# Optimization experiments

Hardware: AMD Instinct MI355X
Metric: run time of the kernel (lower is better)

Reference implementation:

```python
import jax, jax.numpy as jnp
import numpy as np

EMBED_DIM = 1024
HEAD_DIM = 128

def setup_inputs() -> dict:
    key = jax.random.key(0)
    ks = jax.random.split(key, 7)
    B, S = 4, 2048
    x = jax.random.normal(ks[0], (B, S, EMBED_DIM), dtype=jnp.float32)
    # Linear params: weight [embed_dim, head_dim] (applied as x @ W + b), scaled init
    scale = 1.0 / np.sqrt(EMBED_DIM)
    Wq = jax.random.normal(ks[1], (EMBED_DIM, HEAD_DIM), dtype=jnp.float32) * scale
    Wk = jax.random.normal(ks[2], (EMBED_DIM, HEAD_DIM), dtype=jnp.float32) * scale
    Wv = jax.random.normal(ks[3], (EMBED_DIM, HEAD_DIM), dtype=jnp.float32) * scale
    bq = jax.random.normal(ks[4], (HEAD_DIM,), dtype=jnp.float32) * 0.01
    bk = jax.random.normal(ks[5], (HEAD_DIM,), dtype=jnp.float32) * 0.01
    bv = jax.random.normal(ks[6], (HEAD_DIM,), dtype=jnp.float32) * 0.01
    return {"x": x, "Wq": Wq, "bq": bq, "Wk": Wk, "bk": bk, "Wv": Wv, "bv": bv}

def reference(x, Wq, bq, Wk, bk, Wv, bv):
    # x: [B, S, E]
    S = x.shape[1]
    norm = jnp.asarray(HEAD_DIM ** 0.5, x.dtype)
    q = x @ Wq + bq  # [B, S, D]
    k = x @ Wk + bk
    v = x @ Wv + bv
    scores = jnp.einsum('bsd,btd->bst', q, k) / norm  # [B, S, S]
    causal = jnp.tril(jnp.ones((S, S), dtype=bool))
    scores = jnp.where(causal, scores, -jnp.inf)
    att = jax.nn.softmax(scores, axis=-1)
    return jnp.einsum('bst,btd->bsd', att, v)  # [B, S, D]
```

## Files before the change

kernel.cpp:

```cpp
#include <hip/hip_runtime.h>
#include <hip/hip_bf16.h>

typedef __attribute__((ext_vector_type(8))) short short8;
typedef __attribute__((ext_vector_type(4))) float f32x4;

static __device__ __forceinline__ unsigned short f2bf(float f){
  union { float f; unsigned int u; } v; v.f = f;
  unsigned int r = v.u + 0x7fffu + ((v.u >> 16) & 1u);
  return (unsigned short)(r >> 16);
}

static __device__ __forceinline__ void load_lds16(const unsigned short* g, unsigned short* l){
  __builtin_amdgcn_global_load_lds(
      (const __attribute__((address_space(1))) unsigned int*)(g),
      (__attribute__((address_space(3))) unsigned int*)(l), 16, 0, 0);
}

__global__ void k_cvt_x(const float* __restrict__ x, unsigned short* __restrict__ xb){
  int i = (blockIdx.x * 256 + threadIdx.x) * 8;
  float4 a = *(const float4*)(x + i);
  float4 b = *(const float4*)(x + i + 4);
  unsigned short h[8];
  h[0]=f2bf(a.x); h[1]=f2bf(a.y); h[2]=f2bf(a.z); h[3]=f2bf(a.w);
  h[4]=f2bf(b.x); h[5]=f2bf(b.y); h[6]=f2bf(b.z); h[7]=f2bf(b.w);
  *(uint4*)(xb + i) = *(uint4*)h;
}

__global__ void k_prep_w(const float* __restrict__ Wq, const float* __restrict__ Wk,
                         const float* __restrict__ Wv,
                         const float* __restrict__ bq, const float* __restrict__ bk,
                         const float* __restrict__ bv,
                         unsigned short* __restrict__ Wt, float* __restrict__ bias){
  int gid = blockIdx.x * 256 + threadIdx.x;
  int p = gid >> 17;
  int rem = gid & 131071;
  int d = rem >> 10, e = rem & 1023;
  const float* W = (p==0) ? Wq : ((p==1) ? Wk : Wv);
  Wt[gid] = f2bf(W[e*128 + d]);
  if (gid < 384){
    int pp = gid >> 7, dd = gid & 127;
    bias[gid] = (pp==0) ? bq[dd] : ((pp==1) ? bk[dd] : bv[dd]);
  }
}

__global__ __launch_bounds__(256) void k_gemm_qkv(
    const unsigned short* __restrict__ Xb, const unsigned short* __restrict__ Wt,
    float* __restrict__ Cp){
  __shared__ __align__(16) unsigned short As[128*64];
  __shared__ __align__(16) unsigned short Bs[128*64];
  int tid = threadIdx.x;
  int m0 = blockIdx.x * 128;
  int p  = blockIdx.y;
  int kh = blockIdx.z;
  int w = tid >> 6, lane = tid & 63, quad = lane >> 4, l16 = lane & 15;
  int wm = (w >> 1) * 64, wn = (w & 1) * 64;
  f32x4 acc[4][4];
  #pragma unroll
  for (int i=0;i<4;i++)
    #pragma unroll
    for (int j=0;j<4;j++) acc[i][j] = (f32x4){0.f,0.f,0.f,0.f};

  const unsigned short* Wp = Wt + p * (128*1024);
  int rowbase = w * 32;
  const unsigned short* Ag = Xb + (m0 + rowbase + (lane>>3))*1024 + (lane&7)*8;
  const unsigned short* Bg = Wp + (rowbase + (lane>>3))*1024 + (lane&7)*8;
  unsigned short* Al = As + rowbase*64;
  unsigned short* Bl = Bs + rowbase*64;

  int kbeg = kh*512, kend = kbeg + 512;
  for (int k0 = kbeg; k0 < kend; k0 += 64){
    #pragma unroll
    for (int s8=0; s8<4; s8++){
      load_lds16(Ag + k0 + s8*8192, Al + s8*512);
      load_lds16(Bg + k0 + s8*8192, Bl + s8*512);
    }
    __syncthreads();
    #pragma unroll
    for (int kk=0; kk<64; kk+=32){
      short8 af[4], bf[4];
      #pragma unroll
      for (int i=0;i<4;i++) af[i] = *(const short8*)(As + (wm + i*16 + l16)*64 + kk + quad*8);
      #pragma unroll
      for (int j=0;j<4;j++) bf[j] = *(const short8*)(Bs + (wn + j*16 + l16)*64 + kk + quad*8);
      #pragma unroll
      for (int i=0;i<4;i++)
        #pragma unroll
        for (int j=0;j<4;j++)
          acc[i][j] = __builtin_amdgcn_mfma_f32_16x16x32_bf16(af[i], bf[j], acc[i][j], 0,0,0);
    }
    __syncthreads();
  }
  float* slot = Cp + (size_t)(((p*64 + blockIdx.x)*2 + kh)) * 16384;
  #pragma unroll
  for (int i=0;i<4;i++)
    #pragma unroll
    for (int j=0;j<4;j++)
      #pragma unroll
      for (int r=0;r<4;r++)
        slot[(wm + i*16 + quad*4 + r)*128 + wn + j*16 + l16] = acc[i][j][r];
}

__global__ __launch_bounds__(256) void k_gcomb(const float* __restrict__ Cp,
    const float* __restrict__ bias,
    unsigned short* __restrict__ Qsw, unsigned short* __restrict__ Ksw,
    unsigned short* __restrict__ Vsw){
  int mt = blockIdx.x, p = blockIdx.y, tid = threadIdx.x;
  const float* c0p = Cp + (size_t)((p*64+mt)*2) * 16384;
  const float* c1p = c0p + 16384;
  int m0 = mt*128;
  const float qscale = 0.08838834764831845f;
  if (p < 2){
    unsigned short* dst = (p==0)? Qsw : Ksw;
    float scale = (p==0)? qscale : 1.0f;
    for (int it=0; it<16; it++){
      int g = it*256 + tid;
      int row = g >> 5, cs = (g & 31)*4;
      f32x4 a = *(const f32x4*)(c0p + row*128 + cs);
      f32x4 bb = *(const f32x4*)(c1p + row*128 + cs);
      int grow = m0 + row;
      int rt = grow >> 4, m = grow & 15;
      int kc = cs >> 5, q2 = (cs >> 3) & 3, jj = cs & 7;
      unsigned short pk[4];
      #pragma unroll
      for (int k=0;k<4;k++) pk[k] = f2bf((a[k]+bb[k]+bias[p*128+cs+k])*scale);
      *(uint2*)(dst + rt*2048 + kc*512 + q2*128 + m*8 + jj) = *(uint2*)pk;
    }
  } else {
    for (int it=0; it<16; it++){
      int g = it*256 + tid;
      int col = g & 127, rg = g >> 7;
      int r0 = rg*4;
      float bv_ = bias[256 + col];
      unsigned short pk[4];
      #pragma unroll
      for (int k=0;k<4;k++){
        int row = r0 + k;
        pk[k] = f2bf(c0p[row*128+col] + c1p[row*128+col] + bv_);
      }
      int grow0 = m0 + r0;
      int bb2 = grow0 >> 11, s = grow0 & 2047;
      int t64 = s >> 6, srem = s & 63;
      int kc2 = srem >> 5, q2 = (srem >> 3) & 3, jj = srem & 7;
      int nt = col >> 4, l2 = col & 15;
      *(uint2*)(Vsw + (bb2*32+t64)*8192 + nt*1024 + kc2*512 + q2*128 + l2*8 + jj) = *(uint2*)pk;
    }
  }
}

__global__ __launch_bounds__(64) void k_attn(
    const unsigned short* __restrict__ Qsw, const unsigned short* __restrict__ Ksw,
    const unsigned short* __restrict__ Vsw, float* __restrict__ Apart){
  __shared__ __align__(16) unsigned short Pw[2*16*80];
  int x = blockIdx.x;
  int b = x & 3;
  int t = x >> 2;
  int c = t & 7;
  int qb = 63 - (t >> 3);
  int T32 = (qb >> 1) + 1;
  int nch = (T32 + 3) >> 2;
  if (c >= nch) return;
  int lane = threadIdx.x;
  int quad = lane >> 4, l16 = lane & 15;
  int q0 = qb * 32;

  short8 aq[2][4];
  #pragma unroll
  for (int s=0;s<2;s++)
    #pragma unroll
    for (int kc=0;kc<4;kc++)
      aq[s][kc] = *(const short8*)(Qsw + (b*128 + qb*2 + s)*2048 + kc*512 + lane*8);

  f32x4 o[2][8];
  #pragma unroll
  for (int s=0;s<2;s++)
    #pragma unroll
    for (int i=0;i<8;i++) o[s][i] = (f32x4){0.f,0.f,0.f,0.f};
  float mcol[2] = {-1e30f,-1e30f};
  float lcol[2] = {0.f,0.f};
  short8 ap[2][2];

  const unsigned short* Kb = Ksw + b*128*2048;
  const unsigned short* Vb = Vsw + b*32*8192;

  int tEnd = (T32 < c*4+4) ? T32 : (c*4+4);
  for (int tt = c*4; tt < tEnd; tt++){
    int t0 = tt * 64;
    f32x4 sc[2][4];
    #pragma unroll
    for (int s=0;s<2;s++)
      #pragma unroll
      for (int nt=0;nt<4;nt++) sc[s][nt] = (f32x4){0.f,0.f,0.f,0.f};
    #pragma unroll
    for (int nt=0;nt<4;nt++){
      const unsigned short* Kt = Kb + ((t0>>4)+nt)*2048 + lane*8;
      #pragma unroll
      for (int kc=0;kc<4;kc++){
        short8 kf = *(const short8*)(Kt + kc*512);
        sc[0][nt] = __builtin_amdgcn_mfma_f32_16x16x32_bf16(kf, aq[0][kc], sc[0][nt], 0,0,0);
        sc[1][nt] = __builtin_amdgcn_mfma_f32_16x16x32_bf16(kf, aq[1][kc], sc[1][nt], 0,0,0);
      }
    }
    #pragma unroll
    for (int s=0;s<2;s++){
      int qs = q0 + s*16;
      if (t0 + 63 > qs){
        #pragma unroll
        for (int nt=0;nt<4;nt++){
          int kb_ = t0 + nt*16 + quad*4;
          #pragma unroll
          for (int r=0;r<4;r++)
            if (kb_ + r > qs + l16) sc[s][nt][r] = -1e30f;
        }
      }
      float mt_ = -1e30f;
      #pragma unroll
      for (int nt=0;nt<4;nt++)
        #pragma unroll
        for (int r=0;r<4;r++) mt_ = fmaxf(mt_, sc[s][nt][r]);
      mt_ = fmaxf(mt_, __shfl_xor(mt_, 16));
      mt_ = fmaxf(mt_, __shfl_xor(mt_, 32));
      float mn = fmaxf(mcol[s], mt_);
      float al = __expf(mcol[s] - mn);
      mcol[s] = mn;
      float ls = 0.f;
      #pragma unroll
      for (int nt=0;nt<4;nt++)
        #pragma unroll
        for (int r=0;r<4;r++){
          float pv = __expf(sc[s][nt][r] - mn);
          sc[s][nt][r] = pv;
          ls += pv;
        }
      ls += __shfl_xor(ls, 16);
      ls += __shfl_xor(ls, 32);
      lcol[s] = lcol[s]*al + ls;
      #pragma unroll
      for (int r=0;r<4;r++){
        float ar = __shfl(al, quad*4 + r);
        #pragma unroll
        for (int nt=0;nt<8;nt++) o[s][nt][r] *= ar;
      }
      unsigned short* Pws = Pw + s*1280;
      #pragma unroll
      for (int nt=0;nt<4;nt++){
        unsigned short pk[4];
        #pragma unroll
        for (int r=0;r<4;r++) pk[r] = f2bf(sc[s][nt][r]);
        *(uint2*)(Pws + l16*80 + nt*16 + quad*4) = *(uint2*)pk;
      }
      ap[s][0] = *(const short8*)(Pws + l16*80 + quad*8);
      ap[s][1] = *(const short8*)(Pws + l16*80 + 32 + quad*8);
    }
    const unsigned short* Vt0 = Vb + (t0>>6)*8192 + lane*8;
    #pragma unroll
    for (int nt=0; nt<8; nt++)
      #pragma unroll
      for (int kc2=0;kc2<2;kc2++){
        short8 vf = *(const short8*)(Vt0 + nt*1024 + kc2*512);
        o[0][nt] = __builtin_amdgcn_mfma_f32_16x16x32_bf16(ap[0][kc2], vf, o[0][nt], 0,0,0);
        o[1][nt] = __builtin_amdgcn_mfma_f32_16x16x32_bf16(ap[1][kc2], vf, o[1][nt], 0,0,0);
      }
  }

  float* slot = Apart + (size_t)(((b*64 + qb)*8 + c)) * 4160;
  #pragma unroll
  for (int s=0;s<2;s++){
    #pragma unroll
    for (int nt=0;nt<8;nt++)
      #pragma unroll
      for (int r=0;r<4;r++)
        slot[(s*16 + quad*4 + r)*128 + nt*16 + l16] = o[s][nt][r];
    if (quad == 0){
      slot[4096 + s*16 + l16] = mcol[s];
      slot[4128 + s*16 + l16] = lcol[s];
    }
  }
}

__global__ __launch_bounds__(256) void k_acomb(const float* __restrict__ Apart,
                                               float* __restrict__ out){
  int b = blockIdx.x & 3, qb = blockIdx.x >> 2;
  int T32 = (qb >> 1) + 1;
  int nch = (T32 + 3) >> 2;
  const float* base = Apart + (size_t)((b*64 + qb)*8) * 4160;
  int tid = threadIdx.x;
  int row = tid >> 3;
  int c0 = (tid & 7) * 16;
  float m = -1e30f;
  for (int c=0;c<nch;c++) m = fmaxf(m, base[c*4160 + 4096 + row]);
  f32x4 acc[4];
  #pragma unroll
  for (int g=0;g<4;g++) acc[g] = (f32x4){0.f,0.f,0.f,0.f};
  float lsum = 0.f;
  for (int c=0;c<nch;c++){
    float e = __expf(base[c*4160 + 4096 + row] - m);
    lsum += base[c*4160 + 4128 + row] * e;
    #pragma unroll
    for (int g=0;g<4;g++){
      f32x4 v = *(const f32x4*)(base + c*4160 + row*128 + c0 + g*4);
      acc[g] += v * e;
    }
  }
  float inv = 1.0f / lsum;
  float* op = out + (size_t)(b*2048 + qb*32 + row)*128 + c0;
  #pragma unroll
  for (int g=0;g<4;g++){
    f32x4 r = acc[g] * inv;
    *(f32x4*)(op + g*4) = r;
  }
}

extern "C" void kernel_launch(void* const* d_in, const int* in_sizes, int n_in,
                              void* d_out, int out_size, void* d_ws, size_t ws_size,
                              hipStream_t stream) {
  const float* x  = (const float*)d_in[0];
  const float* Wq = (const float*)d_in[1];
  const float* bq = (const float*)d_in[2];
  const float* Wk = (const float*)d_in[3];
  const float* bk = (const float*)d_in[4];
  const float* Wv = (const float*)d_in[5];
  const float* bv = (const float*)d_in[6];
  char* ws = (char*)d_ws;
  unsigned short* Xb   = (unsigned short*)(ws);
  unsigned short* Wt   = (unsigned short*)(ws + 16777216);
  float*          bias = (float*)(ws + 17563648);
  unsigned short* Qsw  = (unsigned short*)(ws + 17565184);
  unsigned short* Ksw  = (unsigned short*)(ws + 19662336);
  unsigned short* Vsw  = (unsigned short*)(ws + 21759488);
  float*          Cp   = (float*)(ws + 23856640);
  float*          Apart= (float*)(ws + 49022464);
  float* out = (float*)d_out;

  hipLaunchKernelGGL(k_cvt_x,   dim3(4096),    dim3(256), 0, stream, x, Xb);
  hipLaunchKernelGGL(k_prep_w,  dim3(1536),    dim3(256), 0, stream, Wq, Wk, Wv, bq, bk, bv, Wt, bias);
  hipLaunchKernelGGL(k_gemm_qkv,dim3(64,3,2),  dim3(256), 0, stream, Xb, Wt, Cp);
  hipLaunchKernelGGL(k_gcomb,   dim3(64,3),    dim3(256), 0, stream, Cp, bias, Qsw, Ksw, Vsw);
  hipLaunchKernelGGL(k_attn,    dim3(2048),    dim3(64),  0, stream, Qsw, Ksw, Vsw, Apart);
  hipLaunchKernelGGL(k_acomb,   dim3(256),     dim3(256), 0, stream, Apart, out);
}
```

Measured before the change: 140.5 us.

## Fuse prep kernels and QKV GEMM epilogue, drop split-K, add MFMA priority

Merges the x conversion and weight prep into one launch. The QKV GEMM is restructured to 64-row tiles with the full K range, so there are no split-K partials. It writes the bias-added, swizzled bf16 Q/K/V directly, which removes the fp32 partial buffer round trip and the separate combine kernel. The attention kernel also raises wave priority around its MFMA blocks via s_setprio. The trade is a longer K loop per block with no split-K parallelism, plus an LDS-staged epilogue.

```diff
diff --git a/kernel.cpp b/kernel.cpp
--- a/kernel.cpp
+++ b/kernel.cpp
@@ -16,133 +16,128 @@
       (__attribute__((address_space(3))) unsigned int*)(l), 16, 0, 0);
 }
 
-__global__ void k_cvt_x(const float* __restrict__ x, unsigned short* __restrict__ xb){
-  int i = (blockIdx.x * 256 + threadIdx.x) * 8;
-  float4 a = *(const float4*)(x + i);
-  float4 b = *(const float4*)(x + i + 4);
-  unsigned short h[8];
-  h[0]=f2bf(a.x); h[1]=f2bf(a.y); h[2]=f2bf(a.z); h[3]=f2bf(a.w);
-  h[4]=f2bf(b.x); h[5]=f2bf(b.y); h[6]=f2bf(b.z); h[7]=f2bf(b.w);
-  *(uint4*)(xb + i) = *(uint4*)h;
-}
-
-__global__ void k_prep_w(const float* __restrict__ Wq, const float* __restrict__ Wk,
-                         const float* __restrict__ Wv,
-                         const float* __restrict__ bq, const float* __restrict__ bk,
-                         const float* __restrict__ bv,
-                         unsigned short* __restrict__ Wt, float* __restrict__ bias){
-  int gid = blockIdx.x * 256 + threadIdx.x;
-  int p = gid >> 17;
-  int rem = gid & 131071;
-  int d = rem >> 10, e = rem & 1023;
-  const float* W = (p==0) ? Wq : ((p==1) ? Wk : Wv);
-  Wt[gid] = f2bf(W[e*128 + d]);
-  if (gid < 384){
-    int pp = gid >> 7, dd = gid & 127;
-    bias[gid] = (pp==0) ? bq[dd] : ((pp==1) ? bk[dd] : bv[dd]);
+__global__ void k_prep(const float* __restrict__ x, unsigned short* __restrict__ xb,
+                       const float* __restrict__ Wq, const float* __restrict__ Wk,
+                       const float* __restrict__ Wv,
+                       const float* __restrict__ bq, const float* __restrict__ bk,
+                       const float* __restrict__ bv,
+                       unsigned short* __restrict__ Wt, float* __restrict__ bias){
+  int bx = blockIdx.x;
+  int tid = threadIdx.x;
+  if (bx < 4096){
+    int i = (bx * 256 + tid) * 8;
+    float4 a = *(const float4*)(x + i);
+    float4 b = *(const float4*)(x + i + 4);
+    unsigned short h[8];
+    h[0]=f2bf(a.x); h[1]=f2bf(a.y); h[2]=f2bf(a.z); h[3]=f2bf(a.w);
+    h[4]=f2bf(b.x); h[5]=f2bf(b.y); h[6]=f2bf(b.z); h[7]=f2bf(b.w);
+    *(uint4*)(xb + i) = *(uint4*)h;
+  } else {
+    int gid = (bx - 4096) * 256 + tid;
+    int p = gid >> 17;
+    int rem = gid & 131071;
+    int d = rem >> 10, e = rem & 1023;
+    const float* W = (p==0) ? Wq : ((p==1) ? Wk : Wv);
+    Wt[gid] = f2bf(W[e*128 + d]);
+    if (gid < 384){
+      int pp = gid >> 7, dd = gid & 127;
+      bias[gid] = (pp==0) ? bq[dd] : ((pp==1) ? bk[dd] : bv[dd]);
+    }
   }
 }
 
 __global__ __launch_bounds__(256) void k_gemm_qkv(
     const unsigned short* __restrict__ Xb, const unsigned short* __restrict__ Wt,
-    float* __restrict__ Cp){
-  __shared__ __align__(16) unsigned short As[128*64];
-  __shared__ __align__(16) unsigned short Bs[128*64];
-  int tid = threadIdx.x;
-  int m0 = blockIdx.x * 128;
-  int p  = blockIdx.y;
-  int kh = blockIdx.z;
-  int w = tid >> 6, lane = tid & 63, quad = lane >> 4, l16 = lane & 15;
-  int wm = (w >> 1) * 64, wn = (w & 1) * 64;
-  f32x4 acc[4][4];
-  #pragma unroll
-  for (int i=0;i<4;i++)
-    #pragma unroll
-    for (int j=0;j<4;j++) acc[i][j] = (f32x4){0.f,0.f,0.f,0.f};
-
-  const unsigned short* Wp = Wt + p * (128*1024);
-  int rowbase = w * 32;
-  const unsigned short* Ag = Xb + (m0 + rowbase + (lane>>3))*1024 + (lane&7)*8;
-  const unsigned short* Bg = Wp + (rowbase + (lane>>3))*1024 + (lane&7)*8;
-  unsigned short* Al = As + rowbase*64;
-  unsigned short* Bl = Bs + rowbase*64;
-
-  int kbeg = kh*512, kend = kbeg + 512;
-  for (int k0 = kbeg; k0 < kend; k0 += 64){
-    #pragma unroll
-    for (int s8=0; s8<4; s8++){
-      load_lds16(Ag + k0 + s8*8192, Al + s8*512);
-      load_lds16(Bg + k0 + s8*8192, Bl + s8*512);
-    }
-    __syncthreads();
-    #pragma unroll
-    for (int kk=0; kk<64; kk+=32){
-      short8 af[4], bf[4];
-      #pragma unroll
-      for (int i=0;i<4;i++) af[i] = *(const short8*)(As + (wm + i*16 + l16)*64 + kk + quad*8);
-      #pragma unroll
-      for (int j=0;j<4;j++) bf[j] = *(const short8*)(Bs + (wn + j*16 + l16)*64 + kk + quad*8);
-      #pragma unroll
-      for (int i=0;i<4;i++)
-        #pragma unroll
-        for (int j=0;j<4;j++)
-          acc[i][j] = __builtin_amdgcn_mfma_f32_16x16x32_bf16(af[i], bf[j], acc[i][j], 0,0,0);
-    }
-    __syncthreads();
-  }
-  float* slot = Cp + (size_t)(((p*64 + blockIdx.x)*2 + kh)) * 16384;
-  #pragma unroll
-  for (int i=0;i<4;i++)
-    #pragma unroll
-    for (int j=0;j<4;j++)
-      #pragma unroll
-      for (int r=0;r<4;r++)
-        slot[(wm + i*16 + quad*4 + r)*128 + wn + j*16 + l16] = acc[i][j][r];
-}
-
-__global__ __launch_bounds__(256) void k_gcomb(const float* __restrict__ Cp,
     const float* __restrict__ bias,
     unsigned short* __restrict__ Qsw, unsigned short* __restrict__ Ksw,
     unsigned short* __restrict__ Vsw){
-  int mt = blockIdx.x, p = blockIdx.y, tid = threadIdx.x;
-  const float* c0p = Cp + (size_t)((p*64+mt)*2) * 16384;
-  const float* c1p = c0p + 16384;
-  int m0 = mt*128;
+  __shared__ __align__(16) char smem[32768];
+  unsigned short* As = (unsigned short*)smem;
+  unsigned short* Bs = (unsigned short*)(smem + 8192);
+  float* Lf = (float*)smem;
+  int tid = threadIdx.x;
+  int mt = blockIdx.x;
+  int p  = blockIdx.y;
+  int m0 = mt * 64;
+  int w = tid >> 6, lane = tid & 63, quad = lane >> 4, l16 = lane & 15;
+  int wm = (w >> 1) * 32, wn = (w & 1) * 64;
+  f32x4 acc[2][4];
+  #pragma unroll
+  for (int i=0;i<2;i++)
+    #pragma unroll
+    for (int j=0;j<4;j++) acc[i][j] = (f32x4){0.f,0.f,0.f,0.f};
+
+  const unsigned short* Wp = Wt + p * (128*1024);
+  const unsigned short* Ag = Xb + (m0 + w*16 + (lane>>3))*1024 + (lane&7)*8;
+  const unsigned short* Bg = Wp + (w*32 + (lane>>3))*1024 + (lane&7)*8;
+  unsigned short* Al = As + (w*16)*64;
+  unsigned short* Bl = Bs + (w*32)*64;
+
+  for (int k0 = 0; k0 < 1024; k0 += 64){
+    #pragma unroll
+    for (int s8=0; s8<2; s8++)
+      load_lds16(Ag + k0 + s8*8192, Al + s8*512);
+    #pragma unroll
+    for (int s8=0; s8<4; s8++)
+      load_lds16(Bg + k0 + s8*8192, Bl + s8*512);
+    __syncthreads();
+    #pragma unroll
+    for (int kk=0; kk<64; kk+=32){
+      short8 af[2], bf[4];
+      #pragma unroll
+      for (int i=0;i<2;i++) af[i] = *(const short8*)(As + (wm + i*16 + l16)*64 + kk + quad*8);
+      #pragma unroll
+      for (int j=0;j<4;j++) bf[j] = *(const short8*)(Bs + (wn + j*16 + l16)*64 + kk + quad*8);
+      #pragma unroll
+      for (int i=0;i<2;i++)
+        #pragma unroll
+        for (int j=0;j<4;j++)
+          acc[i][j] = __builtin_amdgcn_mfma_f32_16x16x32_bf16(af[i], bf[j], acc[i][j], 0,0,0);
+    }
+    __syncthreads();
+  }
+
   const float qscale = 0.08838834764831845f;
-  if (p < 2){
+  if (p == 2){
+    #pragma unroll
+    for (int i=0;i<2;i++)
+      #pragma unroll
+      for (int j=0;j<4;j++){
+        int grow0 = m0 + wm + i*16 + quad*4;
+        int col = wn + j*16 + l16;
+        unsigned short pk[4];
+        float bv_ = bias[256 + col];
+        #pragma unroll
+        for (int r=0;r<4;r++) pk[r] = f2bf(acc[i][j][r] + bv_);
+        int bb2 = grow0 >> 11, s = grow0 & 2047;
+        int t64 = s >> 6, srem = s & 63;
+        int kc2 = srem >> 5, q2 = (srem >> 3) & 3, jj = srem & 7;
+        int nt = col >> 4, l2 = col & 15;
+        *(uint2*)(Vsw + (bb2*32+t64)*8192 + nt*1024 + kc2*512 + q2*128 + l2*8 + jj) = *(uint2*)pk;
+      }
+  } else {
+    #pragma unroll
+    for (int i=0;i<2;i++)
+      #pragma unroll
+      for (int j=0;j<4;j++)
+        #pragma unroll
+        for (int r=0;r<4;r++)
+          Lf[(wm + i*16 + quad*4 + r)*128 + wn + j*16 + l16] = acc[i][j][r];
+    __syncthreads();
     unsigned short* dst = (p==0)? Qsw : Ksw;
     float scale = (p==0)? qscale : 1.0f;
-    for (int it=0; it<16; it++){
+    #pragma unroll
+    for (int it=0; it<8; it++){
       int g = it*256 + tid;
       int row = g >> 5, cs = (g & 31)*4;
-      f32x4 a = *(const f32x4*)(c0p + row*128 + cs);
-      f32x4 bb = *(const f32x4*)(c1p + row*128 + cs);
+      f32x4 a = *(const f32x4*)(Lf + row*128 + cs);
       int grow = m0 + row;
       int rt = grow >> 4, m = grow & 15;
       int kc = cs >> 5, q2 = (cs >> 3) & 3, jj = cs & 7;
       unsigned short pk[4];
       #pragma unroll
-      for (int k=0;k<4;k++) pk[k] = f2bf((a[k]+bb[k]+bias[p*128+cs+k])*scale);
+      for (int k=0;k<4;k++) pk[k] = f2bf((a[k] + bias[p*128+cs+k])*scale);
       *(uint2*)(dst + rt*2048 + kc*512 + q2*128 + m*8 + jj) = *(uint2*)pk;
-    }
-  } else {
-    for (int it=0; it<16; it++){
-      int g = it*256 + tid;
-      int col = g & 127, rg = g >> 7;
-      int r0 = rg*4;
-      float bv_ = bias[256 + col];
-      unsigned short pk[4];
-      #pragma unroll
-      for (int k=0;k<4;k++){
-        int row = r0 + k;
-        pk[k] = f2bf(c0p[row*128+col] + c1p[row*128+col] + bv_);
-      }
-      int grow0 = m0 + r0;
-      int bb2 = grow0 >> 11, s = grow0 & 2047;
-      int t64 = s >> 6, srem = s & 63;
-      int kc2 = srem >> 5, q2 = (srem >> 3) & 3, jj = srem & 7;
-      int nt = col >> 4, l2 = col & 15;
-      *(uint2*)(Vsw + (bb2*32+t64)*8192 + nt*1024 + kc2*512 + q2*128 + l2*8 + jj) = *(uint2*)pk;
     }
   }
 }
@@ -190,6 +185,7 @@
     for (int s=0;s<2;s++)
       #pragma unroll
       for (int nt=0;nt<4;nt++) sc[s][nt] = (f32x4){0.f,0.f,0.f,0.f};
+    __builtin_amdgcn_s_setprio(1);
     #pragma unroll
     for (int nt=0;nt<4;nt++){
       const unsigned short* Kt = Kb + ((t0>>4)+nt)*2048 + lane*8;
@@ -200,6 +196,7 @@
         sc[1][nt] = __builtin_amdgcn_mfma_f32_16x16x32_bf16(kf, aq[1][kc], sc[1][nt], 0,0,0);
       }
     }
+    __builtin_amdgcn_s_setprio(0);
     #pragma unroll
     for (int s=0;s<2;s++){
       int qs = q0 + s*16;
@@ -252,6 +249,7 @@
       ap[s][1] = *(const short8*)(Pws + l16*80 + 32 + quad*8);
     }
     const unsigned short* Vt0 = Vb + (t0>>6)*8192 + lane*8;
+    __builtin_amdgcn_s_setprio(1);
     #pragma unroll
     for (int nt=0; nt<8; nt++)
       #pragma unroll
@@ -260,6 +258,7 @@
         o[0][nt] = __builtin_amdgcn_mfma_f32_16x16x32_bf16(ap[0][kc2], vf, o[0][nt], 0,0,0);
         o[1][nt] = __builtin_amdgcn_mfma_f32_16x16x32_bf16(ap[1][kc2], vf, o[1][nt], 0,0,0);
       }
+    __builtin_amdgcn_s_setprio(0);
   }
 
   float* slot = Apart + (size_t)(((b*64 + qb)*8 + c)) * 4160;
@@ -327,14 +326,13 @@
   unsigned short* Qsw  = (unsigned short*)(ws + 17565184);
   unsigned short* Ksw  = (unsigned short*)(ws + 19662336);
   unsigned short* Vsw  = (unsigned short*)(ws + 21759488);
-  float*          Cp   = (float*)(ws + 23856640);
-  float*          Apart= (float*)(ws + 49022464);
+  float*          Apart= (float*)(ws + 23856640);
   float* out = (float*)d_out;
 
-  hipLaunchKernelGGL(k_cvt_x,   dim3(4096),    dim3(256), 0, stream, x, Xb);
-  hipLaunchKernelGGL(k_prep_w,  dim3(1536),    dim3(256), 0, stream, Wq, Wk, Wv, bq, bk, bv, Wt, bias);
-  hipLaunchKernelGGL(k_gemm_qkv,dim3(64,3,2),  dim3(256), 0, stream, Xb, Wt, Cp);
-  hipLaunchKernelGGL(k_gcomb,   dim3(64,3),    dim3(256), 0, stream, Cp, bias, Qsw, Ksw, Vsw);
+  hipLaunchKernelGGL(k_prep,    dim3(5632),    dim3(256), 0, stream,
+                     x, Xb, Wq, Wk, Wv, bq, bk, bv, Wt, bias);
+  hipLaunchKernelGGL(k_gemm_qkv,dim3(128,3),   dim3(256), 0, stream,
+                     Xb, Wt, bias, Qsw, Ksw, Vsw);
   hipLaunchKernelGGL(k_attn,    dim3(2048),    dim3(64),  0, stream, Qsw, Ksw, Vsw, Apart);
   hipLaunchKernelGGL(k_acomb,   dim3(256),     dim3(256), 0, stream, Apart, out);
 }
```

New measurement: 137.3 us. 1.02x faster.
